# Performance work log

Measured on AMD Instinct MI355X. Metric: run time of the kernel, lower is better.

Reference implementation:

```python
import jax, jax.numpy as jnp
import numpy as np

B, T, HID = 4, 2048, 2048
N_HEAD, N_KV, HD = 16, 2, 128
N_REP = N_HEAD // N_KV


def setup_inputs() -> dict:
    key = jax.random.key(0)
    ks = jax.random.split(key, 7)
    s = 0.02
    return {
        "x": jax.random.normal(ks[0], (B, T, HID), jnp.float32),
        "cos": jax.random.normal(ks[1], (T, 1, HD // 2), jnp.float32),
        "sin": jax.random.normal(ks[2], (T, 1, HD // 2), jnp.float32),
        "Wq": jax.random.normal(ks[3], (N_HEAD * HD, HID), jnp.float32) * s,
        "Wk": jax.random.normal(ks[4], (N_KV * HD, HID), jnp.float32) * s,
        "Wv": jax.random.normal(ks[5], (N_KV * HD, HID), jnp.float32) * s,
        "Wo": jax.random.normal(ks[6], (HID, HID), jnp.float32) * s,
    }


def _rope(x, cos, sin):
    # x: (B, T, H, HD); cos/sin: (T, 1, HD//2) broadcast over B and H
    x_r = x[..., 0::2]
    x_i = x[..., 1::2]
    out_r = x_r * cos - x_i * sin
    out_i = x_r * sin + x_i * cos
    return jnp.stack([out_r, out_i], axis=-1).reshape(x.shape)


def _rms_norm(x):
    eps = jnp.finfo(x.dtype).eps
    var = jnp.mean(jnp.square(x), axis=-1, keepdims=True)
    return x * jax.lax.rsqrt(var + eps)


def reference(x, cos, sin, Wq, Wk, Wv, Wo):
    b, t, _ = x.shape
    q = (x @ Wq.T).reshape(b, t, N_HEAD, HD)
    k = (x @ Wk.T).reshape(b, t, N_KV, HD)
    v = (x @ Wv.T).reshape(b, t, N_KV, HD)
    q = _rms_norm(_rope(q, cos, sin))
    k = _rms_norm(_rope(k, cos, sin))
    # GQA without materializing repeated K/V: group q heads per kv head
    # q: (b, t, n_kv, n_rep, hd) -> (b, n_kv, n_rep, t, hd)
    q = q.reshape(b, t, N_KV, N_REP, HD).transpose(0, 2, 3, 1, 4)
    k = k.transpose(0, 2, 1, 3)  # (b, n_kv, t, hd)
    v = v.transpose(0, 2, 1, 3)
    scale = 1.0 / jnp.sqrt(jnp.asarray(HD, x.dtype))
    scores = jnp.einsum("bgrtd,bgsd->bgrts", q, k) * scale
    causal = jnp.tril(jnp.ones((t, t), dtype=bool))
    scores = jnp.where(causal, scores, jnp.asarray(-jnp.inf, scores.dtype))
    attn = jax.nn.softmax(scores, axis=-1)
    y = jnp.einsum("bgrts,bgsd->bgrtd", attn, v)
    # (b, n_kv, n_rep, t, hd) -> (b, t, n_head*hd)
    y = y.transpose(0, 3, 1, 2, 4).reshape(b, t, N_HEAD * HD)
    return y @ Wo.T
```

## Files before the change

### kernel.cpp

```cpp
#include <hip/hip_runtime.h>

#define B_    4
#define T_    2048
#define HID_  2048
#define NH_   16
#define NKV_  2
#define HD_   128
#define M_    (B_ * T_)
#define NQKV_ 2560

typedef __bf16 bf16x8 __attribute__((ext_vector_type(8)));
typedef float  f32x4  __attribute__((ext_vector_type(4)));

#define AS1 __attribute__((address_space(1)))
#define AS3 __attribute__((address_space(3)))

#if __has_builtin(__builtin_amdgcn_exp2f)
#define EXP2(x) __builtin_amdgcn_exp2f(x)
#else
#define EXP2(x) exp2f(x)
#endif

__device__ __forceinline__ void load_lds16(const void* g, void* l) {
  __builtin_amdgcn_global_load_lds((const AS1 unsigned int*)g,
                                   (AS3 unsigned int*)l, 16, 0, 0);
}

__device__ __forceinline__ unsigned short f2bf(float x) {
  union { float f; unsigned u; } a; a.f = x;
  unsigned r = a.u + 0x7fffu + ((a.u >> 16) & 1u);
  return (unsigned short)(r >> 16);
}
__device__ __forceinline__ float bf2f(unsigned h) {
  union { unsigned u; float f; } a; a.u = h << 16;
  return a.f;
}
__device__ __forceinline__ unsigned pk_rtz(float lo, float hi) {
  union { float f; unsigned u; } a, b; a.f = lo; b.f = hi;
  return (a.u >> 16) | (b.u & 0xffff0000u);
}

__global__ __launch_bounds__(256) void cast_bf16(const float* __restrict__ in,
                                                 unsigned short* __restrict__ out,
                                                 int n4) {
  int i = blockIdx.x * 256 + threadIdx.x;
  if (i >= n4) return;
  float4 v = ((const float4*)in)[i];
  ushort4 o;
  o.x = f2bf(v.x); o.y = f2bf(v.y); o.z = f2bf(v.z); o.w = f2bf(v.w);
  ((ushort4*)out)[i] = o;
}

__global__ __launch_bounds__(256) void cast_w(const float* __restrict__ Wq,
                                              const float* __restrict__ Wk,
                                              const float* __restrict__ Wv,
                                              unsigned short* __restrict__ out) {
  int i = blockIdx.x * 256 + threadIdx.x;
  const float* src; int j;
  if (i < 1048576)      { src = Wq; j = i; }
  else if (i < 1179648) { src = Wk; j = i - 1048576; }
  else                  { src = Wv; j = i - 1179648; }
  float4 v = ((const float4*)src)[j];
  ushort4 o;
  o.x = f2bf(v.x); o.y = f2bf(v.y); o.z = f2bf(v.z); o.w = f2bf(v.w);
  ((ushort4*)out)[i] = o;
}

template <int OUT_BF16>
__global__ __launch_bounds__(256) void gemm_bt(const unsigned short* __restrict__ A,
                                               const unsigned short* __restrict__ Bm,
                                               void* __restrict__ C,
                                               int M, int N, int K) {
  __shared__ __align__(16) unsigned short As[128 * 32];
  __shared__ __align__(16) unsigned short Bs[128 * 32];
  const int tid = threadIdx.x;
  const int w = tid >> 6, lane = tid & 63;
  const int m0 = blockIdx.y << 7, n0 = blockIdx.x << 7;
  const int c = lane & 15, grp = lane >> 4;
  const int lr = lane >> 2;
  const int su = (((lane & 3) ^ ((lr >> 1) & 3)) << 3);
  const int sw = (c >> 1) & 3;
  const int wm = (w & 1) << 6, wn = (w >> 1) << 6;
  f32x4 acc[4][4] = {};
  for (int k0 = 0; k0 < K; k0 += 32) {
    __syncthreads();
    {
      int r0 = w << 4;
      load_lds16(A + (size_t)(m0 + r0 + lr) * K + k0 + su, &As[r0 * 32]);
      load_lds16(A + (size_t)(m0 + 64 + r0 + lr) * K + k0 + su, &As[(64 + r0) * 32]);
      load_lds16(Bm + (size_t)(n0 + r0 + lr) * K + k0 + su, &Bs[r0 * 32]);
      load_lds16(Bm + (size_t)(n0 + 64 + r0 + lr) * K + k0 + su, &Bs[(64 + r0) * 32]);
    }
    __syncthreads();
    bf16x8 af[4], bf[4];
#pragma unroll
    for (int i = 0; i < 4; i++)
      af[i] = *(const bf16x8*)&As[(wm + i * 16 + c) * 32 + ((grp ^ sw) << 3)];
#pragma unroll
    for (int j = 0; j < 4; j++)
      bf[j] = *(const bf16x8*)&Bs[(wn + j * 16 + c) * 32 + ((grp ^ sw) << 3)];
#pragma unroll
    for (int i = 0; i < 4; i++)
#pragma unroll
      for (int j = 0; j < 4; j++)
        acc[i][j] = __builtin_amdgcn_mfma_f32_16x16x32_bf16(af[i], bf[j], acc[i][j], 0, 0, 0);
  }
#pragma unroll
  for (int i = 0; i < 4; i++)
#pragma unroll
    for (int j = 0; j < 4; j++)
#pragma unroll
      for (int r = 0; r < 4; r++) {
        int row = m0 + wm + i * 16 + grp * 4 + r;
        int col = n0 + wn + j * 16 + c;
        float v = acc[i][j][r];
        if (OUT_BF16) ((unsigned short*)C)[(size_t)row * N + col] = f2bf(v);
        else          ((float*)C)[(size_t)row * N + col] = v;
      }
}

__global__ __launch_bounds__(256) void rope_norm(const unsigned short* __restrict__ qkv,
                                                 const float* __restrict__ cosb,
                                                 const float* __restrict__ sinb,
                                                 unsigned short* __restrict__ qo,
                                                 unsigned short* __restrict__ ko,
                                                 unsigned short* __restrict__ vo) {
  const int m = blockIdx.x;
  const int b = m >> 11, t = m & 2047;
  const int w = threadIdx.x >> 6, lane = threadIdx.x & 63;
  const float cv = cosb[t * 64 + lane], sv = sinb[t * 64 + lane];
  const unsigned short* row = qkv + (size_t)m * NQKV_;
  const float QSCL = 0.08838834764831845f * 1.4426950408889634f;
  for (int hh = w; hh < 20; hh += 4) {
    if (hh < 18) {
      const int col0 = (hh < 16) ? hh * 128 : 2048 + (hh - 16) * 128;
      unsigned pr = *(const unsigned*)(row + col0 + 2 * lane);
      float xr = bf2f(pr & 0xffffu), xi = bf2f(pr >> 16);
      float orr = xr * cv - xi * sv;
      float oi  = xr * sv + xi * cv;
      float ss = orr * orr + oi * oi;
#pragma unroll
      for (int off = 1; off < 64; off <<= 1) ss += __shfl_xor(ss, off);
      float scl = rsqrtf(ss * (1.0f / 128.0f) + 1.1920929e-07f);
      if (hh < 16) {
        float s2 = scl * QSCL;
        unsigned out = (unsigned)f2bf(orr * s2) | ((unsigned)f2bf(oi * s2) << 16);
        *(unsigned*)(qo + (((size_t)(b * NH_ + hh)) * T_ + t) * HD_ + 2 * lane) = out;
      } else {
        unsigned out = (unsigned)f2bf(orr * scl) | ((unsigned)f2bf(oi * scl) << 16);
        *(unsigned*)(ko + (((size_t)(b * NKV_ + (hh - 16))) * T_ + t) * HD_ + 2 * lane) = out;
      }
    } else {
      const int gg = hh - 18;
      unsigned pr = *(const unsigned*)(row + 2304 + gg * 128 + 2 * lane);
      *(unsigned*)(vo + (((size_t)(b * NKV_ + gg)) * T_ + t) * HD_ + 2 * lane) = pr;
    }
  }
}

__global__ __launch_bounds__(256) void transpose_v(const unsigned short* __restrict__ v,
                                                   unsigned short* __restrict__ vt) {
  __shared__ unsigned short tile[64][65];
  const int bg = blockIdx.z;
  const int t0 = blockIdx.x << 6, h0 = blockIdx.y << 6;
  const unsigned short* src = v + (size_t)bg * T_ * HD_;
  unsigned short* dst = vt + (size_t)bg * T_ * HD_;
  const int tid = threadIdx.x;
  const int rr = tid >> 4, cc = (tid & 15) << 2;
  const int u = (cc >> 2) & 7;
  const int cp = (cc & 32) + 16 * (u & 1) + 4 * ((u >> 1) & 3);
#pragma unroll
  for (int it = 0; it < 4; it++) {
    int r = rr + it * 16;
    ushort4 d = *(const ushort4*)(src + (size_t)(t0 + r) * HD_ + h0 + cc);
    tile[r][cc + 0] = d.x; tile[r][cc + 1] = d.y;
    tile[r][cc + 2] = d.z; tile[r][cc + 3] = d.w;
  }
  __syncthreads();
#pragma unroll
  for (int it = 0; it < 4; it++) {
    int r = rr + it * 16;
    ushort4 d;
    d.x = tile[cp + 0][r]; d.y = tile[cp + 1][r];
    d.z = tile[cp + 2][r]; d.w = tile[cp + 3][r];
    *(ushort4*)(dst + (size_t)(h0 + r) * T_ + t0 + cc) = d;
  }
}

__global__ __launch_bounds__(256, 2) void flash_attn(const unsigned short* __restrict__ q,
                                                     const unsigned short* __restrict__ k,
                                                     const unsigned short* __restrict__ vt,
                                                     unsigned short* __restrict__ y) {
  __shared__ __align__(16) unsigned short Kb[2][8192];
  __shared__ __align__(16) unsigned short Vb[2][8192];
  const int tid = threadIdx.x;
  const int w = tid >> 6, lane = tid & 63;
  const int c = lane & 15, grp = lane >> 4;
  const int lr = lane >> 2;
  const int sw = (c >> 1) & 3;
  const int su = (((lane & 3) ^ ((lr >> 1) & 3)) << 3);

  const int idx = blockIdx.x;
  const int p  = idx & 7;
  const int hq = (idx >> 3) & 15;
  const int b  = idx >> 7;
  const int g  = hq >> 3;

  const unsigned short* kbase  = k  + ((size_t)(b * NKV_ + g)) * T_ * HD_;
  const unsigned short* vtbase = vt + ((size_t)(b * NKV_ + g)) * HD_ * T_;

  auto stage = [&](int s0, int bb) {
    const unsigned short* kp = kbase + (size_t)(s0 + w * 16 + lr) * HD_ + su;
#pragma unroll
    for (int dc = 0; dc < 4; dc++)
      load_lds16(kp + dc * 32, &Kb[bb][dc * 2048 + (w * 16) * 32]);
    const unsigned short* vp = vtbase + s0 + su;
#pragma unroll
    for (int ks = 0; ks < 2; ks++)
#pragma unroll
      for (int jj = 0; jj < 2; jj++)
        load_lds16(vp + (size_t)(w * 32 + jj * 16 + lr) * T_ + ks * 32,
                   &Vb[bb][ks * 4096 + (w * 32 + jj * 16) * 32]);
  };

  for (int ph = 0; ph < 2; ph++) {
    const int tile = ph ? p : (15 - p);
    const int t0 = tile << 7;
    const int t0w = t0 + w * 32;
    const unsigned short* qbase = q + (((size_t)(b * NH_ + hq)) * T_ + t0) * HD_;

    bf16x8 qf[2][4];
#pragma unroll
    for (int ti = 0; ti < 2; ti++)
#pragma unroll
      for (int ks = 0; ks < 4; ks++)
        qf[ti][ks] = *(const bf16x8*)(qbase + (size_t)(w * 32 + ti * 16 + c) * HD_ + ks * 32 + grp * 8);

    f32x4 oacc[2][8] = {};
    float mrun[2], lrun[2];
    mrun[0] = mrun[1] = -__builtin_inff();
    lrun[0] = lrun[1] = 0.f;

    const int nch = (t0 >> 6) + 2;
    stage(0, 0);
    __syncthreads();
    for (int ic = 0; ic < nch; ic++) {
      const int s0 = ic << 6, bb = ic & 1;
      if (ic + 1 < nch) stage((ic + 1) << 6, bb ^ 1);
      if (s0 <= t0w + 31) {
        const unsigned short* Kc = Kb[bb];
        const unsigned short* Vc = Vb[bb];
        f32x4 st[2][4] = {};
        __builtin_amdgcn_s_setprio(1);
#pragma unroll
        for (int s = 0; s < 4; s++)
#pragma unroll
          for (int kvt = 0; kvt < 4; kvt++) {
            bf16x8 ak = *(const bf16x8*)&Kc[s * 2048 + (kvt * 16 + c) * 32 + ((grp ^ sw) << 3)];
            st[0][kvt] = __builtin_amdgcn_mfma_f32_16x16x32_bf16(ak, qf[0][s], st[0][kvt], 0, 0, 0);
            st[1][kvt] = __builtin_amdgcn_mfma_f32_16x16x32_bf16(ak, qf[1][s], st[1][kvt], 0, 0, 0);
          }
        __builtin_amdgcn_s_setprio(0);
        if (s0 + 63 > t0w) {
#pragma unroll
          for (int ti = 0; ti < 2; ti++)
#pragma unroll
            for (int kvt = 0; kvt < 4; kvt++)
#pragma unroll
              for (int r = 0; r < 4; r++) {
                int kv = s0 + kvt * 16 + grp * 4 + r;
                int qq = t0w + ti * 16 + c;
                if (kv > qq) st[ti][kvt][r] = -__builtin_inff();
              }
        }
        unsigned pkv[2][4][2];
#pragma unroll
        for (int ti = 0; ti < 2; ti++) {
          float rm = st[ti][0][0];
#pragma unroll
          for (int kvt = 0; kvt < 4; kvt++)
#pragma unroll
            for (int r = 0; r < 4; r++) rm = fmaxf(rm, st[ti][kvt][r]);
          rm = fmaxf(rm, __shfl_xor(rm, 16));
          rm = fmaxf(rm, __shfl_xor(rm, 32));
          if (!__all(rm <= mrun[ti] + 8.f)) {
            float mnew = fmaxf(mrun[ti], rm);
            float alpha = EXP2(mrun[ti] - mnew);
            mrun[ti] = mnew;
            lrun[ti] *= alpha;
#pragma unroll
            for (int hj = 0; hj < 8; hj++)
#pragma unroll
              for (int r = 0; r < 4; r++) oacc[ti][hj][r] *= alpha;
          }
          const float m0 = mrun[ti];
          float rs = 0.f;
#pragma unroll
          for (int kvt = 0; kvt < 4; kvt++) {
            float p0 = EXP2(st[ti][kvt][0] - m0);
            float p1 = EXP2(st[ti][kvt][1] - m0);
            float p2 = EXP2(st[ti][kvt][2] - m0);
            float p3 = EXP2(st[ti][kvt][3] - m0);
            rs += (p0 + p1) + (p2 + p3);
            pkv[ti][kvt][0] = pk_rtz(p0, p1);
            pkv[ti][kvt][1] = pk_rtz(p2, p3);
          }
          rs += __shfl_xor(rs, 16);
          rs += __shfl_xor(rs, 32);
          lrun[ti] += rs;
        }
        __builtin_amdgcn_s_setprio(1);
#pragma unroll
        for (int s = 0; s < 2; s++) {
          union { int4 i; bf16x8 v; } pf0, pf1;
          pf0.i = make_int4(pkv[0][2 * s][0], pkv[0][2 * s][1], pkv[0][2 * s + 1][0], pkv[0][2 * s + 1][1]);
          pf1.i = make_int4(pkv[1][2 * s][0], pkv[1][2 * s][1], pkv[1][2 * s + 1][0], pkv[1][2 * s + 1][1]);
#pragma unroll
          for (int hj = 0; hj < 8; hj++) {
            union { int4 i; bf16x8 v; } av;
            av.i = *(const int4*)&Vc[s * 4096 + (hj * 16 + c) * 32 + ((grp ^ sw) << 3)];
            oacc[0][hj] = __builtin_amdgcn_mfma_f32_16x16x32_bf16(av.v, pf0.v, oacc[0][hj], 0, 0, 0);
            oacc[1][hj] = __builtin_amdgcn_mfma_f32_16x16x32_bf16(av.v, pf1.v, oacc[1][hj], 0, 0, 0);
          }
        }
        __builtin_amdgcn_s_setprio(0);
      }
      __syncthreads();
    }

#pragma unroll
    for (int ti = 0; ti < 2; ti++) {
      float inv = 1.f / lrun[ti];
      int trow = t0 + w * 32 + ti * 16 + c;
#pragma unroll
      for (int hj = 0; hj < 8; hj++) {
        ushort4 o;
        o.x = f2bf(oacc[ti][hj][0] * inv);
        o.y = f2bf(oacc[ti][hj][1] * inv);
        o.z = f2bf(oacc[ti][hj][2] * inv);
        o.w = f2bf(oacc[ti][hj][3] * inv);
        *(ushort4*)&y[((size_t)(b * T_ + trow)) * HID_ + hq * HD_ + hj * 16 + grp * 4] = o;
      }
    }
  }
}

extern "C" void kernel_launch(void* const* d_in, const int* in_sizes, int n_in,
                              void* d_out, int out_size, void* d_ws, size_t ws_size,
                              hipStream_t stream) {
  const float* x    = (const float*)d_in[0];
  const float* cosb = (const float*)d_in[1];
  const float* sinb = (const float*)d_in[2];
  const float* Wq   = (const float*)d_in[3];
  const float* Wk   = (const float*)d_in[4];
  const float* Wv   = (const float*)d_in[5];
  const float* Wo   = (const float*)d_in[6];
  float* out = (float*)d_out;

  char* ws = (char*)d_ws;
  size_t off = 0;
  auto take = [&](size_t elems) {
    unsigned short* p = (unsigned short*)(ws + off);
    off += ((elems * 2 + 255) & ~(size_t)255);
    return p;
  };
  unsigned short* xb   = take((size_t)M_ * HID_);
  unsigned short* wqkv = take((size_t)NQKV_ * HID_);
  unsigned short* wob  = take((size_t)HID_ * HID_);
  unsigned short* qkv  = take((size_t)M_ * NQKV_);
  unsigned short* qb   = take((size_t)B_ * NH_ * T_ * HD_);
  unsigned short* kb   = take((size_t)B_ * NKV_ * T_ * HD_);
  unsigned short* vb   = take((size_t)B_ * NKV_ * T_ * HD_);
  unsigned short* vtb  = take((size_t)B_ * NKV_ * T_ * HD_);
  unsigned short* yb   = take((size_t)M_ * HID_);
  (void)ws_size; (void)in_sizes; (void)n_in; (void)out_size;

  cast_bf16<<<16384, 256, 0, stream>>>(x, xb, 4194304);
  cast_w<<<5120, 256, 0, stream>>>(Wq, Wk, Wv, wqkv);
  cast_bf16<<<4096, 256, 0, stream>>>(Wo, wob, 1048576);

  gemm_bt<1><<<dim3(20, 64), 256, 0, stream>>>(xb, wqkv, qkv, M_, NQKV_, HID_);
  rope_norm<<<8192, 256, 0, stream>>>(qkv, cosb, sinb, qb, kb, vb);
  transpose_v<<<dim3(32, 2, 8), 256, 0, stream>>>(vb, vtb);
  flash_attn<<<dim3(512), 256, 0, stream>>>(qb, kb, vtb, yb);
  gemm_bt<0><<<dim3(16, 64), 256, 0, stream>>>(yb, wob, out, M_, HID_, HID_);
}
```

Measured before the change: 478.3 us.

## Replace GEMM with 256x256-tile, 8-wave, 4-stage pipelined LDS kernel

Replaces the 128x128, 4-wave single-buffered GEMM with a 256x256 tile kernel that uses 8 waves and a 4-deep LDS ring buffer. Global-to-LDS loads are issued three k-tiles ahead and interleaved with MFMA phases, using explicit vmcnt waits, s_barrier and setprio. The goal is to overlap memory latency with compute, raise data reuse per tile, and remove the per-iteration __syncthreads stalls. In exchange it uses 128KB of LDS per block and many more accumulator registers, and the larger tiles give fewer blocks (320 and 256) to spread across CUs.

```diff
diff --git a/kernel.cpp b/kernel.cpp
--- a/kernel.cpp
+++ b/kernel.cpp
@@ -66,54 +66,109 @@
   ((ushort4*)out)[i] = o;
 }
 
+#define GT_VM8  do { asm volatile("s_waitcnt vmcnt(8)" ::: "memory"); __builtin_amdgcn_sched_barrier(0); } while (0)
+#define GT_VM4  do { asm volatile("s_waitcnt vmcnt(4)" ::: "memory"); __builtin_amdgcn_sched_barrier(0); } while (0)
+#define GT_VM0  do { asm volatile("s_waitcnt vmcnt(0)" ::: "memory"); __builtin_amdgcn_sched_barrier(0); } while (0)
+#define GT_NONE ((void)0)
+
+#define GTILE(KT, DOSTAGE, VMW)                                               \
+  {                                                                           \
+    const int cb = (KT) & 3;                                                  \
+    bf16x8 af[4];                                                             \
+    _Pragma("unroll")                                                         \
+    for (int nt = 0; nt < 4; nt++)                                            \
+      bfr[nt] = *(const bf16x8*)&Bs[cb][(wc * 64 + nt * 16 + c) * 32 + rsw];  \
+    _Pragma("unroll")                                                         \
+    for (int mt = 0; mt < 4; mt++)                                            \
+      af[mt] = *(const bf16x8*)&As[cb][(wr * 128 + mt * 16 + c) * 32 + rsw];  \
+    if (DOSTAGE) {                                       \
+      const int sb = ((KT) + 3) & 3;                                          \
+      const unsigned short* ap = A + a_stoff + (size_t)((KT) + 3) * 32;       \
+      load_lds16(ap, &As[sb][(w * 16) * 32]);                                 \
+      load_lds16(ap + (size_t)128 * K, &As[sb][(128 + w * 16) * 32]);         \
+    }                                                                         \
+    __builtin_amdgcn_s_barrier();                                             \
+    __builtin_amdgcn_s_setprio(1);                                            \
+    _Pragma("unroll")                                                         \
+    for (int mt = 0; mt < 4; mt++)                                            \
+      _Pragma("unroll")                                                       \
+      for (int nt = 0; nt < 4; nt++)                                          \
+        acc[mt][nt] = __builtin_amdgcn_mfma_f32_16x16x32_bf16(af[mt], bfr[nt], acc[mt][nt], 0, 0, 0); \
+    __builtin_amdgcn_s_setprio(0);                                            \
+    __builtin_amdgcn_s_barrier();                                             \
+    _Pragma("unroll")                                                         \
+    for (int mt = 0; mt < 4; mt++)                                            \
+      af[mt] = *(const bf16x8*)&As[cb][(wr * 128 + 64 + mt * 16 + c) * 32 + rsw]; \
+    if (DOSTAGE) {                                       \
+      const int sb = ((KT) + 3) & 3;                                          \
+      const unsigned short* bp = Bm + b_stoff + (size_t)((KT) + 3) * 32;      \
+      load_lds16(bp, &Bs[sb][(w * 16) * 32]);                                 \
+      load_lds16(bp + (size_t)128 * K, &Bs[sb][(128 + w * 16) * 32]);         \
+    }                                                                         \
+    VMW;                                                                      \
+    __builtin_amdgcn_s_barrier();                                             \
+    __builtin_amdgcn_s_setprio(1);                                            \
+    _Pragma("unroll")                                                         \
+    for (int mt = 0; mt < 4; mt++)                                            \
+      _Pragma("unroll")                                                       \
+      for (int nt = 0; nt < 4; nt++)                                          \
+        acc[4 + mt][nt] = __builtin_amdgcn_mfma_f32_16x16x32_bf16(af[mt], bfr[nt], acc[4 + mt][nt], 0, 0, 0); \
+    __builtin_amdgcn_s_setprio(0);                                            \
+    __builtin_amdgcn_s_barrier();                                             \
+  }
+
 template <int OUT_BF16>
-__global__ __launch_bounds__(256) void gemm_bt(const unsigned short* __restrict__ A,
-                                               const unsigned short* __restrict__ Bm,
-                                               void* __restrict__ C,
-                                               int M, int N, int K) {
-  __shared__ __align__(16) unsigned short As[128 * 32];
-  __shared__ __align__(16) unsigned short Bs[128 * 32];
+__global__ __launch_bounds__(512, 2) void gemm_bt8(const unsigned short* __restrict__ A,
+                                                   const unsigned short* __restrict__ Bm,
+                                                   void* __restrict__ C,
+                                                   int M, int N, int K) {
+  __shared__ __align__(16) unsigned short As[4][256 * 32];
+  __shared__ __align__(16) unsigned short Bs[4][256 * 32];
   const int tid = threadIdx.x;
   const int w = tid >> 6, lane = tid & 63;
-  const int m0 = blockIdx.y << 7, n0 = blockIdx.x << 7;
+  const int wr = w >> 2, wc = w & 3;
   const int c = lane & 15, grp = lane >> 4;
   const int lr = lane >> 2;
   const int su = (((lane & 3) ^ ((lr >> 1) & 3)) << 3);
-  const int sw = (c >> 1) & 3;
-  const int wm = (w & 1) << 6, wn = (w >> 1) << 6;
-  f32x4 acc[4][4] = {};
-  for (int k0 = 0; k0 < K; k0 += 32) {
-    __syncthreads();
-    {
-      int r0 = w << 4;
-      load_lds16(A + (size_t)(m0 + r0 + lr) * K + k0 + su, &As[r0 * 32]);
-      load_lds16(A + (size_t)(m0 + 64 + r0 + lr) * K + k0 + su, &As[(64 + r0) * 32]);
-      load_lds16(Bm + (size_t)(n0 + r0 + lr) * K + k0 + su, &Bs[r0 * 32]);
-      load_lds16(Bm + (size_t)(n0 + 64 + r0 + lr) * K + k0 + su, &Bs[(64 + r0) * 32]);
+  const int rsw = ((grp ^ ((c >> 1) & 3)) << 3);
+  const int m0 = blockIdx.y << 8, n0 = blockIdx.x << 8;
+
+  const size_t a_stoff = (size_t)(m0 + w * 16 + lr) * K + su;
+  const size_t b_stoff = (size_t)(n0 + w * 16 + lr) * K + su;
+
+  f32x4 acc[8][4] = {};
+  bf16x8 bfr[4];
+  const int nkt = K >> 5;
+
+  {
+#pragma unroll
+    for (int kt = 0; kt < 3; kt++) {
+      const unsigned short* ap = A + a_stoff + (size_t)kt * 32;
+      load_lds16(ap, &As[kt][(w * 16) * 32]);
+      load_lds16(ap + (size_t)128 * K, &As[kt][(128 + w * 16) * 32]);
+      const unsigned short* bp = Bm + b_stoff + (size_t)kt * 32;
+      load_lds16(bp, &Bs[kt][(w * 16) * 32]);
+      load_lds16(bp + (size_t)128 * K, &Bs[kt][(128 + w * 16) * 32]);
     }
-    __syncthreads();
-    bf16x8 af[4], bf[4];
-#pragma unroll
-    for (int i = 0; i < 4; i++)
-      af[i] = *(const bf16x8*)&As[(wm + i * 16 + c) * 32 + ((grp ^ sw) << 3)];
-#pragma unroll
-    for (int j = 0; j < 4; j++)
-      bf[j] = *(const bf16x8*)&Bs[(wn + j * 16 + c) * 32 + ((grp ^ sw) << 3)];
-#pragma unroll
-    for (int i = 0; i < 4; i++)
-#pragma unroll
-      for (int j = 0; j < 4; j++)
-        acc[i][j] = __builtin_amdgcn_mfma_f32_16x16x32_bf16(af[i], bf[j], acc[i][j], 0, 0, 0);
-  }
-#pragma unroll
-  for (int i = 0; i < 4; i++)
-#pragma unroll
-    for (int j = 0; j < 4; j++)
+    GT_VM8;
+    __builtin_amdgcn_s_barrier();
+  }
+
+  for (int kt = 0; kt + 3 < nkt; ++kt)
+    GTILE(kt, 1, GT_VM8)
+  GTILE(nkt - 3, 0, GT_VM4)
+  GTILE(nkt - 2, 0, GT_VM0)
+  GTILE(nkt - 1, 0, GT_NONE)
+
+#pragma unroll
+  for (int mt = 0; mt < 8; mt++)
+#pragma unroll
+    for (int nt = 0; nt < 4; nt++)
 #pragma unroll
       for (int r = 0; r < 4; r++) {
-        int row = m0 + wm + i * 16 + grp * 4 + r;
-        int col = n0 + wn + j * 16 + c;
-        float v = acc[i][j][r];
+        int row = m0 + wr * 128 + (mt >> 2) * 64 + (mt & 3) * 16 + grp * 4 + r;
+        int col = n0 + wc * 64 + nt * 16 + c;
+        float v = acc[mt][nt][r];
         if (OUT_BF16) ((unsigned short*)C)[(size_t)row * N + col] = f2bf(v);
         else          ((float*)C)[(size_t)row * N + col] = v;
       }
@@ -379,9 +434,9 @@
   cast_w<<<5120, 256, 0, stream>>>(Wq, Wk, Wv, wqkv);
   cast_bf16<<<4096, 256, 0, stream>>>(Wo, wob, 1048576);
 
-  gemm_bt<1><<<dim3(20, 64), 256, 0, stream>>>(xb, wqkv, qkv, M_, NQKV_, HID_);
+  gemm_bt8<1><<<dim3(10, 32), 512, 0, stream>>>(xb, wqkv, qkv, M_, NQKV_, HID_);
   rope_norm<<<8192, 256, 0, stream>>>(qkv, cosb, sinb, qb, kb, vb);
   transpose_v<<<dim3(32, 2, 8), 256, 0, stream>>>(vb, vtb);
   flash_attn<<<dim3(512), 256, 0, stream>>>(qb, kb, vtb, yb);
-  gemm_bt<0><<<dim3(16, 64), 256, 0, stream>>>(yb, wob, out, M_, HID_, HID_);
-}
+  gemm_bt8<0><<<dim3(8, 32), 512, 0, stream>>>(yb, wob, out, M_, HID_, HID_);
+}
```

After: 459.9 us. 1.04x faster.

## Replace 128x128 GEMM with 256x256 double-buffered pipelined 8-wave GEMM

Applied to the files above, without the earlier changes.

Replaces the simple 128x128 tile GEMM, which loads and then syncs on every K step, with a 256x256 tile over 8 waves and K=64 steps. LDS is double-buffered, and global-to-LDS loads for the next two K tiles are interleaved with MFMA phases using barriers, vmcnt waits and setprio. The aim is more data reuse per tile and hiding memory latency behind compute in both the QKV and output projections. The cost is fewer blocks (320 and 256 on a 256-CU device, so under two waves), 128KB of LDS, and high register pressure at one block per CU.

```diff
diff --git a/kernel.cpp b/kernel.cpp
--- a/kernel.cpp
+++ b/kernel.cpp
@@ -67,53 +67,109 @@
 }
 
 template <int OUT_BF16>
-__global__ __launch_bounds__(256) void gemm_bt(const unsigned short* __restrict__ A,
-                                               const unsigned short* __restrict__ Bm,
-                                               void* __restrict__ C,
-                                               int M, int N, int K) {
-  __shared__ __align__(16) unsigned short As[128 * 32];
-  __shared__ __align__(16) unsigned short Bs[128 * 32];
+__global__ __launch_bounds__(512, 1) void gemm256(const unsigned short* __restrict__ A,
+                                                  const unsigned short* __restrict__ Bm,
+                                                  void* __restrict__ C,
+                                                  int M, int N, int K) {
+  __shared__ __align__(16) unsigned short As[2][16384];
+  __shared__ __align__(16) unsigned short Bs[2][16384];
   const int tid = threadIdx.x;
   const int w = tid >> 6, lane = tid & 63;
-  const int m0 = blockIdx.y << 7, n0 = blockIdx.x << 7;
+  const int wr = w >> 2, wc = w & 3;
   const int c = lane & 15, grp = lane >> 4;
-  const int lr = lane >> 2;
-  const int su = (((lane & 3) ^ ((lr >> 1) & 3)) << 3);
-  const int sw = (c >> 1) & 3;
-  const int wm = (w & 1) << 6, wn = (w >> 1) << 6;
-  f32x4 acc[4][4] = {};
-  for (int k0 = 0; k0 < K; k0 += 32) {
-    __syncthreads();
-    {
-      int r0 = w << 4;
-      load_lds16(A + (size_t)(m0 + r0 + lr) * K + k0 + su, &As[r0 * 32]);
-      load_lds16(A + (size_t)(m0 + 64 + r0 + lr) * K + k0 + su, &As[(64 + r0) * 32]);
-      load_lds16(Bm + (size_t)(n0 + r0 + lr) * K + k0 + su, &Bs[r0 * 32]);
-      load_lds16(Bm + (size_t)(n0 + 64 + r0 + lr) * K + k0 + su, &Bs[(64 + r0) * 32]);
+  const int c7 = c & 7;
+  const int m0 = blockIdx.y << 8, n0 = blockIdx.x << 8;
+  const int srow = w * 8 + (lane >> 3);
+  const int su = ((lane & 7) ^ ((lane >> 3) & 7)) << 3;
+
+  f32x4 acc[8][4] = {};
+  const int nkt = K >> 6;
+
+  auto stA = [&](int h, int kt, int db) {
+    const unsigned short* p = A + (size_t)(m0 + h * 128 + srow) * K + kt * 64 + su;
+    load_lds16(p, &As[db][h * 8192 + (w * 8) * 64]);
+    load_lds16(p + (size_t)64 * K, &As[db][h * 8192 + (64 + w * 8) * 64]);
+  };
+  auto stB = [&](int h, int kt, int db) {
+    const unsigned short* p = Bm + (size_t)(n0 + h * 128 + srow) * K + kt * 64 + su;
+    load_lds16(p, &Bs[db][h * 8192 + (w * 8) * 64]);
+    load_lds16(p + (size_t)64 * K, &Bs[db][h * 8192 + (64 + w * 8) * 64]);
+  };
+
+  stA(0, 0, 0); stA(1, 0, 0); stB(0, 0, 0); stB(1, 0, 0);
+  if (nkt > 1) { stB(0, 1, 1); stB(1, 1, 1); stA(0, 1, 1); }
+  asm volatile("s_waitcnt vmcnt(6)" ::: "memory");
+  __builtin_amdgcn_s_barrier();
+
+  const int Abase = wr * 8192;
+  const int Bbase = (wc >> 1) * 8192 + ((wc & 1) * 64) * 64;
+
+#define RDQ(arr, mtA, mtB)                                                          \
+  _Pragma("unroll")                                                                 \
+  for (int ks = 0; ks < 2; ks++) {                                                  \
+    arr[0][ks] = *(const bf16x8*)&Ad[((mtA) * 16 + c) * 64 + (((ks << 2) + grp) ^ c7) * 8]; \
+    arr[1][ks] = *(const bf16x8*)&Ad[((mtB) * 16 + c) * 64 + (((ks << 2) + grp) ^ c7) * 8]; \
+  }
+#define MMQ(arr, mt0)                                                               \
+  __builtin_amdgcn_s_setprio(1);                                                    \
+  _Pragma("unroll")                                                                 \
+  for (int i = 0; i < 2; i++)                                                       \
+    _Pragma("unroll")                                                               \
+    for (int nt = 0; nt < 4; nt++)                                                  \
+      _Pragma("unroll")                                                             \
+      for (int ks = 0; ks < 2; ks++)                                                \
+        acc[(mt0) + i][nt] = __builtin_amdgcn_mfma_f32_16x16x32_bf16(               \
+            arr[i][ks], b_[nt][ks], acc[(mt0) + i][nt], 0, 0, 0);                   \
+  __builtin_amdgcn_s_setprio(0);
+
+  for (int kt = 0; kt < nkt; ++kt) {
+    const int db = kt & 1;
+    const unsigned short* Ad = &As[db][Abase];
+    const unsigned short* Bd = &Bs[db][Bbase];
+    bf16x8 b_[4][2], a01[2][2], a23[2][2], a45[2][2], a67[2][2];
+    RDQ(a01, 0, 1)
+#pragma unroll
+    for (int nt = 0; nt < 4; nt++)
+#pragma unroll
+      for (int ks = 0; ks < 2; ks++)
+        b_[nt][ks] = *(const bf16x8*)&Bd[(nt * 16 + c) * 64 + (((ks << 2) + grp) ^ c7) * 8];
+    RDQ(a23, 2, 3)
+    if (kt + 1 < nkt) stA(1, kt + 1, db ^ 1);
+    __builtin_amdgcn_s_barrier();
+    MMQ(a01, 0)
+    __builtin_amdgcn_s_barrier();
+    RDQ(a45, 4, 5)
+    if (kt + 2 < nkt) stB(0, kt + 2, db);
+    __builtin_amdgcn_s_barrier();
+    MMQ(a23, 2)
+    __builtin_amdgcn_s_barrier();
+    RDQ(a67, 6, 7)
+    if (kt + 2 < nkt) stB(1, kt + 2, db);
+    __builtin_amdgcn_s_barrier();
+    MMQ(a45, 4)
+    __builtin_amdgcn_s_barrier();
+    if (kt + 2 < nkt) {
+      stA(0, kt + 2, db);
+      asm volatile("s_waitcnt vmcnt(6)" ::: "memory");
+    } else {
+      asm volatile("s_waitcnt vmcnt(0)" ::: "memory");
     }
-    __syncthreads();
-    bf16x8 af[4], bf[4];
-#pragma unroll
-    for (int i = 0; i < 4; i++)
-      af[i] = *(const bf16x8*)&As[(wm + i * 16 + c) * 32 + ((grp ^ sw) << 3)];
-#pragma unroll
-    for (int j = 0; j < 4; j++)
-      bf[j] = *(const bf16x8*)&Bs[(wn + j * 16 + c) * 32 + ((grp ^ sw) << 3)];
-#pragma unroll
-    for (int i = 0; i < 4; i++)
-#pragma unroll
-      for (int j = 0; j < 4; j++)
-        acc[i][j] = __builtin_amdgcn_mfma_f32_16x16x32_bf16(af[i], bf[j], acc[i][j], 0, 0, 0);
-  }
-#pragma unroll
-  for (int i = 0; i < 4; i++)
-#pragma unroll
-    for (int j = 0; j < 4; j++)
+    __builtin_amdgcn_s_barrier();
+    MMQ(a67, 6)
+    __builtin_amdgcn_s_barrier();
+  }
+#undef RDQ
+#undef MMQ
+
+#pragma unroll
+  for (int mt = 0; mt < 8; mt++)
+#pragma unroll
+    for (int nt = 0; nt < 4; nt++)
 #pragma unroll
       for (int r = 0; r < 4; r++) {
-        int row = m0 + wm + i * 16 + grp * 4 + r;
-        int col = n0 + wn + j * 16 + c;
-        float v = acc[i][j][r];
+        int row = m0 + wr * 128 + mt * 16 + grp * 4 + r;
+        int col = n0 + wc * 64 + nt * 16 + c;
+        float v = acc[mt][nt][r];
         if (OUT_BF16) ((unsigned short*)C)[(size_t)row * N + col] = f2bf(v);
         else          ((float*)C)[(size_t)row * N + col] = v;
       }
@@ -379,9 +435,9 @@
   cast_w<<<5120, 256, 0, stream>>>(Wq, Wk, Wv, wqkv);
   cast_bf16<<<4096, 256, 0, stream>>>(Wo, wob, 1048576);
 
-  gemm_bt<1><<<dim3(20, 64), 256, 0, stream>>>(xb, wqkv, qkv, M_, NQKV_, HID_);
+  gemm256<1><<<dim3(10, 32), 512, 0, stream>>>(xb, wqkv, qkv, M_, NQKV_, HID_);
   rope_norm<<<8192, 256, 0, stream>>>(qkv, cosb, sinb, qb, kb, vb);
   transpose_v<<<dim3(32, 2, 8), 256, 0, stream>>>(vb, vtb);
   flash_attn<<<dim3(512), 256, 0, stream>>>(qb, kb, vtb, yb);
-  gemm_bt<0><<<dim3(16, 64), 256, 0, stream>>>(yb, wob, out, M_, HID_, HID_);
-}
+  gemm256<0><<<dim3(8, 32), 512, 0, stream>>>(yb, wob, out, M_, HID_, HID_);
+}
```

After: 459.0 us. 1.04x faster.
